# Kernel optimization log

Measured on AMD Instinct MI355X. Metric: run time of the kernel, lower is better.

## Reference

```python
import jax, jax.numpy as jnp
import numpy as np


def setup_inputs() -> dict:
    key = jax.random.key(0)
    k1, k2 = jax.random.split(key)
    B, L, D = 8, 4096, 64
    x = jax.random.normal(k1, (B, L, D), dtype=jnp.float32)
    # per-token validity mask [B, L, 1] with 0/1 entries (outer product builds the pairwise mask)
    mask = jax.random.randint(k2, (B, L, 1), 0, 2, dtype=jnp.int32)
    return {"x": x, "mask": mask}


def reference(x, mask):
    # OriAttention with head=1: q = k = v = x, shapes [B, L, D]
    B, L, D = x.shape
    scale = D ** 0.25  # note: fourth root of d, as in the original
    scores = jnp.einsum('bqd,bkd->bqk', x, x) / scale  # [B, L, L]
    # pairwise mask via outer product of the [B, L, 1] token mask, then bool cast
    mf = mask.astype(jnp.float32)
    pair = jnp.matmul(mf, mf.transpose(0, 2, 1)) != 0.0  # [B, L, L] bool
    scores = jnp.where(pair, scores, jnp.float32(-10000000.0))
    # original softmaxes along dim=2 of [B, H, Lq, Lk], i.e. over the QUERY axis
    attn = jax.nn.softmax(scores, axis=1)  # normalize over q for each k
    # then transposes (2,3) and matmuls with v: out[b,k,:] = sum_q attn[b,q,k] * v[b,q,:]
    out = jnp.einsum('bqk,bqd->bkd', attn, x)  # [B, L, D]
    return out
```

## Files before the change

kernel.cpp:

```cpp
#include <hip/hip_runtime.h>
#include <stdint.h>

typedef __attribute__((ext_vector_type(8))) __bf16 bf16x8;
typedef __attribute__((ext_vector_type(4))) __bf16 bf16x4;
typedef __attribute__((ext_vector_type(4))) float f32x4;

#define MFMA_BF16(A, B, C) __builtin_amdgcn_mfma_f32_16x16x32_bf16((A), (B), (C), 0, 0, 0)
#define VBAR() asm volatile("s_waitcnt vmcnt(0) lgkmcnt(0)\ns_barrier" ::: "memory")

__device__ __forceinline__ void gload16(const void* g, void* l) {
  __builtin_amdgcn_global_load_lds((const __attribute__((address_space(1))) void*)g,
                                   (__attribute__((address_space(3))) void*)l, 16, 0, 0);
}

namespace {

constexpr int kBatch = 8;
constexpr int kL = 4096;
constexpr int kD = 64;
constexpr int kQB = 128;
constexpr int kKB = 64;
constexpr int kSlotPad = 4096;
constexpr int kMaxTiles = 64;
constexpr int kSlotCap = 2304;
constexpr int kSplits = 8;
constexpr float kC = 1.4426950408889634f / 2.8284271247461903f;

constexpr size_t kWsPartialOff = 0;
constexpr size_t kWsCountOff = 65536;
constexpr size_t kWsIdxOff = 65600;
constexpr size_t kWsRankOff = 131136;
constexpr size_t kWsPlOff = 196672;
constexpr size_t kWsXchOff = 1376320;
constexpr size_t kWsVtgOff = 5570624;
constexpr size_t kWsPaccOff = 9764928;

__device__ __forceinline__ int fk(int r) { return (r & 3) | ((r >> 1) & 4); }

__device__ __forceinline__ size_t slotrow(int s, int b, int slot, bool fb) {
  return fb ? ((size_t)b * kL + slot) : ((size_t)(s * kBatch + b) * kSlotCap + slot);
}

__global__ void k_pre(const float* __restrict__ x, const int* __restrict__ mask,
                      float* __restrict__ partial, uint16_t* __restrict__ idx,
                      uint16_t* __restrict__ rank, int* __restrict__ counts) {
  const int b = blockIdx.y;
  const int bx = blockIdx.x;
  const int t = threadIdx.x;
  __shared__ float sm[256];
  __shared__ int wcnt[4];
  __shared__ int woff[5];

  if (bx < 32) {
    const int d = t & 63, rs = t >> 6;
    const float* xb = x + (size_t)b * kL * kD;
    float s = 0.0f;
    const int r0 = bx * 128 + rs;
    for (int i = 0; i < 32; ++i) s += xb[(size_t)(r0 + i * 4) * kD + d];
    sm[t] = s;
    __syncthreads();
    if (t < 64) partial[(b * 32 + bx) * 64 + t] = sm[t] + sm[t + 64] + sm[t + 128] + sm[t + 192];
  } else {
    const int wave = t >> 6, lane = t & 63;
    const int* mb = mask + b * kL;
    const int base = wave * 1024;
    int local = 0;
    for (int rnd = 0; rnd < 16; ++rnd)
      local += __popcll(__ballot(mb[base + rnd * 64 + lane] != 0));
    if (lane == 0) wcnt[wave] = local;
    __syncthreads();
    if (t == 0) {
      woff[0] = 0;
      for (int w = 0; w < 4; ++w) woff[w + 1] = woff[w] + wcnt[w];
      counts[b] = woff[4];
    }
    __syncthreads();
    int pos = woff[wave];
    uint16_t* ib = idx + b * kL;
    uint16_t* rb = rank + b * kL;
    for (int rnd = 0; rnd < 16; ++rnd) {
      const int k = base + rnd * 64 + lane;
      const bool m = (mb[k] != 0);
      const unsigned long long bal = __ballot(m);
      const int p = pos + __popcll(bal & ((1ull << lane) - 1ull));
      if (m) { ib[p] = (uint16_t)k; rb[k] = (uint16_t)p; }
      pos += __popcll(bal);
    }
  }
}

__global__ __launch_bounds__(256) void k_conv(const float* __restrict__ x,
                                              const uint16_t* __restrict__ idx,
                                              const int* __restrict__ counts,
                                              __bf16* __restrict__ xch,
                                              __bf16* __restrict__ vtg) {
  const int b = blockIdx.x;
  const int tile = blockIdx.y;
  const int count = counts[b];
  const int NT = (count + kKB - 1) >> 6;
  if (tile >= NT) return;
  const int t = threadIdx.x;
  const int srow = t >> 2, q3 = t & 3;
  const int slot = tile * kKB + srow;
  __shared__ __align__(16) __bf16 tmp[kKB][80];

  float v16[16];
  if (slot < count) {
    const int rowi = idx[b * kL + slot];
    const float4* p = (const float4*)(x + ((size_t)b * kL + rowi) * kD + q3 * 16);
    const float4 a0 = p[0], a1 = p[1], a2 = p[2], a3 = p[3];
    v16[0] = a0.x; v16[1] = a0.y; v16[2] = a0.z; v16[3] = a0.w;
    v16[4] = a1.x; v16[5] = a1.y; v16[6] = a1.z; v16[7] = a1.w;
    v16[8] = a2.x; v16[9] = a2.y; v16[10] = a2.z; v16[11] = a2.w;
    v16[12] = a3.x; v16[13] = a3.y; v16[14] = a3.z; v16[15] = a3.w;
  } else {
#pragma unroll
    for (int i = 0; i < 16; ++i) v16[i] = 0.0f;
  }
  bf16x8 u0, u1;
#pragma unroll
  for (int j = 0; j < 8; ++j) { u0[j] = (__bf16)v16[j]; u1[j] = (__bf16)v16[8 + j]; }

  {
    __bf16* xrow = xch + ((size_t)b * kSlotPad + slot) * kD;
    const int f = fk(srow);
    *(bf16x8*)(xrow + (((2 * q3) ^ f) << 3)) = u0;
    *(bf16x8*)(xrow + (((2 * q3 + 1) ^ f) << 3)) = u1;
  }
  *(bf16x8*)&tmp[srow][q3 * 16] = u0;
  *(bf16x8*)&tmp[srow][q3 * 16 + 8] = u1;
  __syncthreads();
  {
    const int d = t >> 2, kq = t & 3;
    bf16x8 c0, c1;
#pragma unroll
    for (int i = 0; i < 8; ++i) {
      c0[i] = tmp[kq * 16 + i][d];
      c1[i] = tmp[kq * 16 + 8 + i][d];
    }
    __bf16* vrow = vtg + (((size_t)b * kMaxTiles + tile) * kKB + d) * kD;
    const int e = d & 7;
    *(bf16x8*)(vrow + (((2 * kq) ^ e) << 3)) = c0;
    *(bf16x8*)(vrow + (((2 * kq + 1) ^ e) << 3)) = c1;
  }
}

__global__ __launch_bounds__(256, 4) void k_attn(const __bf16* __restrict__ xch,
                                                 const __bf16* __restrict__ vtg,
                                                 const int* __restrict__ counts,
                                                 float* __restrict__ pl,
                                                 __bf16* __restrict__ pacc) {
  const int b = blockIdx.x;
  const int s = blockIdx.y;
  const int qt = blockIdx.z;

  int cmax = 0;
#pragma unroll
  for (int i = 0; i < kBatch; ++i) cmax = max(cmax, counts[i]);
  const bool fb = cmax > kSlotCap;
  const int nS = fb ? 1 : (int)gridDim.y;
  if (fb && s > 0) return;

  const int count = counts[b];
  if (qt * kQB >= count) return;
  const int NTtot = (count + kKB - 1) >> 6;
  const int TPS = (NTtot + nS - 1) / nS;
  const int t0 = s * TPS;
  const int t1 = min(NTtot, t0 + TPS);

  const int tid = threadIdx.x;
  const int wave = tid >> 6;
  const int lane = tid & 63;
  const int lg = lane >> 4;
  const int lr = lane & 15;

  int qpos[2];
  bool qvalid[2];
  size_t sr[2];
#pragma unroll
  for (int h = 0; h < 2; ++h) {
    qpos[h] = qt * kQB + h * 64 + wave * 16 + lr;
    qvalid[h] = qpos[h] < count;
    sr[h] = slotrow(s, b, qpos[h], fb);
  }

  if (t0 >= t1) {
#pragma unroll
    for (int h = 0; h < 2; ++h) {
      if (qvalid[h]) {
        const bf16x4 z = (bf16x4)(__bf16)0.0f;
#pragma unroll
        for (int dt = 0; dt < 4; ++dt) *(bf16x4*)&pacc[sr[h] * kD + dt * 16 + lg * 4] = z;
        if (lg == 0) pl[sr[h]] = 0.0f;
      }
    }
    return;
  }

  const __bf16* __restrict__ xb = xch + (size_t)b * kSlotPad * kD;
  const __bf16* __restrict__ vb = vtg + (size_t)b * kMaxTiles * (kKB * kD);

  __shared__ __align__(16) __bf16 KhB[2][kKB * kD];
  __shared__ __align__(16) __bf16 VtB[2][kKB * kD];

  bf16x8 qh[2][2];
#pragma unroll
  for (int h = 0; h < 2; ++h) {
    const int qr = qvalid[h] ? qpos[h] : 0;
    const __bf16* qrow = xb + (size_t)qr * kD;
    const int f = fk(qr & 63);
#pragma unroll
    for (int kt = 0; kt < 2; ++kt)
      qh[h][kt] = *(const bf16x8*)(qrow + (((kt * 4 + lg) ^ f) << 3));
  }

  f32x4 acc[2][4];
#pragma unroll
  for (int h = 0; h < 2; ++h)
#pragma unroll
    for (int i = 0; i < 4; ++i) acc[h][i] = (f32x4)0.0f;
  float l_run[2] = {0.0f, 0.0f};

  auto stage = [&](int t, int buf) {
    const size_t goff = (size_t)t * (kKB * kD);
    const int lo = lane * 8;
#pragma unroll
    for (int c = 0; c < 2; ++c) {
      const int eo = wave * 1024 + c * 512;
      gload16(xb + goff + eo + lo, &KhB[buf][eo]);
      gload16(vb + goff + eo + lo, &VtB[buf][eo]);
    }
  };

  stage(t0, 0);
  VBAR();

  int cur = 0;
  for (int t = t0; t < t1; ++t) {
    const bool havenext = (t + 1 < t1);
    if (havenext) stage(t + 1, cur ^ 1);

    const __bf16* Kh = &KhB[cur][0];
    const __bf16* Vt = &VtB[cur][0];

    f32x4 S_[2][2][2];
#pragma unroll
    for (int g = 0; g < 2; ++g) {
#pragma unroll
      for (int tt = 0; tt < 2; ++tt) {
        const int krow = g * 32 + ((lr >> 2) << 3) + tt * 4 + (lr & 3);
        const int f = fk(krow);
        f32x4 s0 = (f32x4)0.0f, s1 = (f32x4)0.0f;
#pragma unroll
        for (int kt = 0; kt < 2; ++kt) {
          const bf16x8 ah = *(const bf16x8*)&Kh[(krow << 6) + (((kt * 4 + lg) ^ f) << 3)];
          s0 = MFMA_BF16(ah, qh[0][kt], s0);
          s1 = MFMA_BF16(ah, qh[1][kt], s1);
        }
        S_[0][g][tt] = s0;
        S_[1][g][tt] = s1;
      }
    }

    float p[2][2][2][4];
#pragma unroll
    for (int h = 0; h < 2; ++h)
#pragma unroll
      for (int g = 0; g < 2; ++g)
#pragma unroll
        for (int tt = 0; tt < 2; ++tt)
#pragma unroll
          for (int r = 0; r < 4; ++r)
            p[h][g][tt][r] = __builtin_amdgcn_exp2f(S_[h][g][tt][r] * kC);

    if (t == NTtot - 1 && (count & 63)) {
      const int valid = count & 63;
#pragma unroll
      for (int h = 0; h < 2; ++h)
#pragma unroll
        for (int g = 0; g < 2; ++g)
#pragma unroll
          for (int tt = 0; tt < 2; ++tt)
#pragma unroll
            for (int r = 0; r < 4; ++r) {
              const int kl2 = g * 32 + lg * 8 + tt * 4 + r;
              if (kl2 >= valid) p[h][g][tt][r] = 0.0f;
            }
    }

#pragma unroll
    for (int h = 0; h < 2; ++h) {
      float lt = 0.0f;
#pragma unroll
      for (int g = 0; g < 2; ++g)
#pragma unroll
        for (int tt = 0; tt < 2; ++tt)
#pragma unroll
          for (int r = 0; r < 4; ++r) lt += p[h][g][tt][r];
      lt += __shfl_xor(lt, 16);
      lt += __shfl_xor(lt, 32);
      l_run[h] += lt;
    }

    bf16x8 pf[2][2];
#pragma unroll
    for (int h = 0; h < 2; ++h)
#pragma unroll
      for (int g = 0; g < 2; ++g)
#pragma unroll
        for (int tt = 0; tt < 2; ++tt)
#pragma unroll
          for (int r = 0; r < 4; ++r) pf[h][g][tt * 4 + r] = (__bf16)p[h][g][tt][r];

#pragma unroll
    for (int g = 0; g < 2; ++g) {
#pragma unroll
      for (int dt = 0; dt < 4; ++dt) {
        const int d = dt * 16 + lr;
        const bf16x8 vf =
            *(const bf16x8*)&Vt[(d << 6) + ((((g << 2) + lg) ^ (d & 7)) << 3)];
        acc[0][dt] = MFMA_BF16(vf, pf[0][g], acc[0][dt]);
        acc[1][dt] = MFMA_BF16(vf, pf[1][g], acc[1][dt]);
      }
    }

    if (havenext) VBAR();
    cur ^= 1;
  }

#pragma unroll
  for (int h = 0; h < 2; ++h) {
    if (qvalid[h]) {
#pragma unroll
      for (int dt = 0; dt < 4; ++dt) {
        bf16x4 v;
#pragma unroll
        for (int r = 0; r < 4; ++r) v[r] = (__bf16)acc[h][dt][r];
        *(bf16x4*)&pacc[sr[h] * kD + dt * 16 + lg * 4] = v;
      }
      if (lg == 0) pl[sr[h]] = l_run[h];
    }
  }
}

template <int TS>
__global__ __launch_bounds__(256) void k_post(const int* __restrict__ mask,
                                              const float* __restrict__ partial,
                                              const uint16_t* __restrict__ rank,
                                              const int* __restrict__ counts,
                                              const float* __restrict__ pl,
                                              const __bf16* __restrict__ pacc,
                                              float* __restrict__ out) {
  const int b = blockIdx.y;
  const int c = blockIdx.x;
  const int t = threadIdx.x;

  int cmax = 0;
#pragma unroll
  for (int i = 0; i < kBatch; ++i) cmax = max(cmax, counts[i]);
  const bool fb = cmax > kSlotCap;

  __shared__ float mean[64];
  __shared__ float winv[32];
  __shared__ int slotL[32];

  if (t < 64) {
    float s = 0.0f;
    for (int p = 0; p < 32; ++p) s += partial[(b * 32 + p) * 64 + t];
    mean[t] = s * (1.0f / (float)kL);
  } else if (t < 96) {
    const int i = t - 64;
    const int r = c * 32 + i;
    if (mask[b * kL + r] == 0) {
      slotL[i] = -1;
    } else {
      const int slot = rank[b * kL + r];
      slotL[i] = slot;
      float L = 0.0f;
      if (!fb) {
#pragma unroll
        for (int s2 = 0; s2 < TS; ++s2)
          L += pl[(size_t)(s2 * kBatch + b) * kSlotCap + slot];
      } else {
        L = pl[(size_t)b * kL + slot];
      }
      winv[i] = 1.0f / L;
    }
  }
  __syncthreads();

  const int d = t & 63;
#pragma unroll
  for (int it = 0; it < 8; ++it) {
    const int rl = it * 4 + (t >> 6);
    const int slot = slotL[rl];
    float o;
    if (slot < 0) {
      o = mean[d];
    } else if (!fb) {
      o = 0.0f;
#pragma unroll
      for (int s2 = 0; s2 < TS; ++s2)
        o += (float)pacc[((size_t)(s2 * kBatch + b) * kSlotCap + slot) * kD + d];
      o *= winv[rl];
    } else {
      o = winv[rl] * (float)pacc[((size_t)b * kL + slot) * kD + d];
    }
    out[((size_t)b * kL + c * 32 + rl) * kD + d] = o;
  }
}

}

extern "C" void kernel_launch(void* const* d_in, const int* in_sizes, int n_in,
                              void* d_out, int out_size, void* d_ws, size_t ws_size,
                              hipStream_t stream) {
  const float* x = (const float*)d_in[0];
  const int* mask = (const int*)d_in[1];
  float* out = (float*)d_out;
  char* ws = (char*)d_ws;
  float* partial = (float*)(ws + kWsPartialOff);
  int* counts = (int*)(ws + kWsCountOff);
  uint16_t* idx = (uint16_t*)(ws + kWsIdxOff);
  uint16_t* rank = (uint16_t*)(ws + kWsRankOff);
  float* pl = (float*)(ws + kWsPlOff);
  __bf16* xch = (__bf16*)(ws + kWsXchOff);
  __bf16* vtg = (__bf16*)(ws + kWsVtgOff);
  __bf16* pacc = (__bf16*)(ws + kWsPaccOff);

  int S = kSplits;
  while (S > 1 && ws_size < kWsPaccOff + (size_t)S * kBatch * kSlotCap * kD * 2) S >>= 1;

  k_pre<<<dim3(33, kBatch), dim3(256), 0, stream>>>(x, mask, partial, idx, rank, counts);
  k_conv<<<dim3(kBatch, kMaxTiles), dim3(256), 0, stream>>>(x, idx, counts, xch, vtg);
  k_attn<<<dim3(kBatch, S, kL / kQB), dim3(256), 0, stream>>>(xch, vtg, counts, pl, pacc);
  switch (S) {
    case 8:
      k_post<8><<<dim3(128, kBatch), dim3(256), 0, stream>>>(mask, partial, rank, counts,
                                                             pl, pacc, out);
      break;
    case 4:
      k_post<4><<<dim3(128, kBatch), dim3(256), 0, stream>>>(mask, partial, rank, counts,
                                                             pl, pacc, out);
      break;
    case 2:
      k_post<2><<<dim3(128, kBatch), dim3(256), 0, stream>>>(mask, partial, rank, counts,
                                                             pl, pacc, out);
      break;
    default:
      k_post<1><<<dim3(128, kBatch), dim3(256), 0, stream>>>(mask, partial, rank, counts,
                                                             pl, pacc, out);
      break;
  }
}
```

Before: 42.14 us.

## Fuse mask compaction into conversion kernel and compute row sums via MFMA

```diff
diff --git a/kernel.cpp b/kernel.cpp
--- a/kernel.cpp
+++ b/kernel.cpp
@@ -28,7 +28,6 @@
 
 constexpr size_t kWsPartialOff = 0;
 constexpr size_t kWsCountOff = 65536;
-constexpr size_t kWsIdxOff = 65600;
 constexpr size_t kWsRankOff = 131136;
 constexpr size_t kWsPlOff = 196672;
 constexpr size_t kWsXchOff = 1376320;
@@ -41,72 +40,83 @@
   return fb ? ((size_t)b * kL + slot) : ((size_t)(s * kBatch + b) * kSlotCap + slot);
 }
 
-__global__ void k_pre(const float* __restrict__ x, const int* __restrict__ mask,
-                      float* __restrict__ partial, uint16_t* __restrict__ idx,
-                      uint16_t* __restrict__ rank, int* __restrict__ counts) {
+__global__ __launch_bounds__(256) void k_prep(const float* __restrict__ x,
+                                              const int* __restrict__ mask,
+                                              float* __restrict__ partial,
+                                              uint16_t* __restrict__ rank,
+                                              int* __restrict__ counts,
+                                              __bf16* __restrict__ xch,
+                                              __bf16* __restrict__ vtg) {
   const int b = blockIdx.y;
   const int bx = blockIdx.x;
   const int t = threadIdx.x;
-  __shared__ float sm[256];
-  __shared__ int wcnt[4];
-  __shared__ int woff[5];
-
-  if (bx < 32) {
+
+  if (bx >= 64) {
+    const int part = bx - 64;
+    __shared__ float sm[256];
     const int d = t & 63, rs = t >> 6;
     const float* xb = x + (size_t)b * kL * kD;
     float s = 0.0f;
-    const int r0 = bx * 128 + rs;
+    const int r0 = part * 128 + rs;
     for (int i = 0; i < 32; ++i) s += xb[(size_t)(r0 + i * 4) * kD + d];
     sm[t] = s;
     __syncthreads();
-    if (t < 64) partial[(b * 32 + bx) * 64 + t] = sm[t] + sm[t + 64] + sm[t + 128] + sm[t + 192];
-  } else {
-    const int wave = t >> 6, lane = t & 63;
-    const int* mb = mask + b * kL;
-    const int base = wave * 1024;
-    int local = 0;
-    for (int rnd = 0; rnd < 16; ++rnd)
-      local += __popcll(__ballot(mb[base + rnd * 64 + lane] != 0));
-    if (lane == 0) wcnt[wave] = local;
+    if (t < 64)
+      partial[(b * 32 + part) * 64 + t] = sm[t] + sm[t + 64] + sm[t + 128] + sm[t + 192];
+    return;
+  }
+
+  __shared__ int scan[256];
+  __shared__ int slotTab[64];
+  __shared__ __align__(16) __bf16 tmp[kKB][80];
+
+  const int* mb = mask + b * kL;
+  const int r0 = t * 16;
+  int msk16 = 0, cnt = 0;
+#pragma unroll
+  for (int i = 0; i < 16; ++i) {
+    if (mb[r0 + i] != 0) { msk16 |= 1 << i; ++cnt; }
+  }
+  scan[t] = cnt;
+  if (t < 64) slotTab[t] = -1;
+  __syncthreads();
+#pragma unroll
+  for (int off = 1; off < 256; off <<= 1) {
+    const int v = (t >= off) ? scan[t - off] : 0;
     __syncthreads();
-    if (t == 0) {
-      woff[0] = 0;
-      for (int w = 0; w < 4; ++w) woff[w + 1] = woff[w] + wcnt[w];
-      counts[b] = woff[4];
-    }
+    scan[t] += v;
     __syncthreads();
-    int pos = woff[wave];
-    uint16_t* ib = idx + b * kL;
-    uint16_t* rb = rank + b * kL;
-    for (int rnd = 0; rnd < 16; ++rnd) {
-      const int k = base + rnd * 64 + lane;
-      const bool m = (mb[k] != 0);
-      const unsigned long long bal = __ballot(m);
-      const int p = pos + __popcll(bal & ((1ull << lane) - 1ull));
-      if (m) { ib[p] = (uint16_t)k; rb[k] = (uint16_t)p; }
-      pos += __popcll(bal);
-    }
-  }
-}
-
-__global__ __launch_bounds__(256) void k_conv(const float* __restrict__ x,
-                                              const uint16_t* __restrict__ idx,
-                                              const int* __restrict__ counts,
-                                              __bf16* __restrict__ xch,
-                                              __bf16* __restrict__ vtg) {
-  const int b = blockIdx.x;
-  const int tile = blockIdx.y;
-  const int count = counts[b];
+  }
+  const int count = scan[255];
+  const int base = bx * 64;
+  {
+    int rk = scan[t] - cnt;
+#pragma unroll
+    for (int i = 0; i < 16; ++i) {
+      if (msk16 & (1 << i)) {
+        if (rk >= base && rk < base + 64) slotTab[rk - base] = r0 + i;
+        ++rk;
+      }
+    }
+  }
+  if (bx == 0) {
+    int rk = scan[t] - cnt;
+#pragma unroll
+    for (int i = 0; i < 16; ++i) {
+      if (msk16 & (1 << i)) { rank[b * kL + r0 + i] = (uint16_t)rk; ++rk; }
+    }
+    if (t == 0) counts[b] = count;
+  }
+  __syncthreads();
+
   const int NT = (count + kKB - 1) >> 6;
-  if (tile >= NT) return;
-  const int t = threadIdx.x;
+  if (bx >= NT) return;
+
   const int srow = t >> 2, q3 = t & 3;
-  const int slot = tile * kKB + srow;
-  __shared__ __align__(16) __bf16 tmp[kKB][80];
-
+  const int slot = base + srow;
+  const int rowi = slotTab[srow];
   float v16[16];
-  if (slot < count) {
-    const int rowi = idx[b * kL + slot];
+  if (rowi >= 0) {
     const float4* p = (const float4*)(x + ((size_t)b * kL + rowi) * kD + q3 * 16);
     const float4 a0 = p[0], a1 = p[1], a2 = p[2], a3 = p[3];
     v16[0] = a0.x; v16[1] = a0.y; v16[2] = a0.z; v16[3] = a0.w;
@@ -138,7 +148,7 @@
       c0[i] = tmp[kq * 16 + i][d];
       c1[i] = tmp[kq * 16 + 8 + i][d];
     }
-    __bf16* vrow = vtg + (((size_t)b * kMaxTiles + tile) * kKB + d) * kD;
+    __bf16* vrow = vtg + (((size_t)b * kMaxTiles + bx) * kKB + d) * kD;
     const int e = d & 7;
     *(bf16x8*)(vrow + (((2 * kq) ^ e) << 3)) = c0;
     *(bf16x8*)(vrow + (((2 * kq + 1) ^ e) << 3)) = c1;
@@ -215,11 +225,17 @@
   }
 
   f32x4 acc[2][4];
-#pragma unroll
-  for (int h = 0; h < 2; ++h)
+  f32x4 acc_l[2];
+#pragma unroll
+  for (int h = 0; h < 2; ++h) {
 #pragma unroll
     for (int i = 0; i < 4; ++i) acc[h][i] = (f32x4)0.0f;
-  float l_run[2] = {0.0f, 0.0f};
+    acc_l[h] = (f32x4)0.0f;
+  }
+
+  bf16x8 vone;
+#pragma unroll
+  for (int j = 0; j < 8; ++j) vone[j] = (lr == 0) ? (__bf16)1.0f : (__bf16)0.0f;
 
   auto stage = [&](int t, int buf) {
     const size_t goff = (size_t)t * (kKB * kD);
@@ -288,32 +304,20 @@
             }
     }
 
-#pragma unroll
-    for (int h = 0; h < 2; ++h) {
-      float lt = 0.0f;
+    bf16x8 pf[2][2];
+#pragma unroll
+    for (int h = 0; h < 2; ++h)
 #pragma unroll
       for (int g = 0; g < 2; ++g)
 #pragma unroll
         for (int tt = 0; tt < 2; ++tt)
 #pragma unroll
-          for (int r = 0; r < 4; ++r) lt += p[h][g][tt][r];
-      lt += __shfl_xor(lt, 16);
-      lt += __shfl_xor(lt, 32);
-      l_run[h] += lt;
-    }
-
-    bf16x8 pf[2][2];
-#pragma unroll
-    for (int h = 0; h < 2; ++h)
-#pragma unroll
-      for (int g = 0; g < 2; ++g)
-#pragma unroll
-        for (int tt = 0; tt < 2; ++tt)
-#pragma unroll
           for (int r = 0; r < 4; ++r) pf[h][g][tt * 4 + r] = (__bf16)p[h][g][tt][r];
 
 #pragma unroll
     for (int g = 0; g < 2; ++g) {
+      acc_l[0] = MFMA_BF16(vone, pf[0][g], acc_l[0]);
+      acc_l[1] = MFMA_BF16(vone, pf[1][g], acc_l[1]);
 #pragma unroll
       for (int dt = 0; dt < 4; ++dt) {
         const int d = dt * 16 + lr;
@@ -338,7 +342,7 @@
         for (int r = 0; r < 4; ++r) v[r] = (__bf16)acc[h][dt][r];
         *(bf16x4*)&pacc[sr[h] * kD + dt * 16 + lg * 4] = v;
       }
-      if (lg == 0) pl[sr[h]] = l_run[h];
+      if (lg == 0) pl[sr[h]] = acc_l[h][0];
     }
   }
 }
@@ -421,7 +425,6 @@
   char* ws = (char*)d_ws;
   float* partial = (float*)(ws + kWsPartialOff);
   int* counts = (int*)(ws + kWsCountOff);
-  uint16_t* idx = (uint16_t*)(ws + kWsIdxOff);
   uint16_t* rank = (uint16_t*)(ws + kWsRankOff);
   float* pl = (float*)(ws + kWsPlOff);
   __bf16* xch = (__bf16*)(ws + kWsXchOff);
@@ -431,8 +434,8 @@
   int S = kSplits;
   while (S > 1 && ws_size < kWsPaccOff + (size_t)S * kBatch * kSlotCap * kD * 2) S >>= 1;
 
-  k_pre<<<dim3(33, kBatch), dim3(256), 0, stream>>>(x, mask, partial, idx, rank, counts);
-  k_conv<<<dim3(kBatch, kMaxTiles), dim3(256), 0, stream>>>(x, idx, counts, xch, vtg);
+  k_prep<<<dim3(96, kBatch), dim3(256), 0, stream>>>(x, mask, partial, rank, counts,
+                                                     xch, vtg);
   k_attn<<<dim3(kBatch, S, kL / kQB), dim3(256), 0, stream>>>(xch, vtg, counts, pl, pacc);
   switch (S) {
     case 8:
```

Measured after the change: 40.31 us. 4.3% less time.
